# Performance work log

Measured on AMD Instinct MI355X. Metric: run time of the kernel, lower is better.

Reference implementation:

```python
import jax, jax.numpy as jnp
import numpy as np

EPS = 1e-8
VOX_WIDTH = 1.0
CURV_THRESH = 0.5


def _build_kernels():
    """Nine 3x3x3 central finite-difference stencils, pre-divided by vox_width / vox_width^2."""
    def zk():
        return np.zeros((3, 3, 3), np.float32)
    ks = {}
    # first derivatives (central difference), denominator vox_width
    for name, ax in (('ddx', 0), ('ddy', 1), ('ddz', 2)):
        k = zk(); i = [1, 1, 1]
        i[ax] = 0; k[tuple(i)] = -0.5
        i[ax] = 2; k[tuple(i)] = 0.5
        ks[name] = k / VOX_WIDTH
    # pure second derivatives, denominator vox_width^2
    for name, ax in (('d2dx2', 0), ('d2dy2', 1), ('d2dz2', 2)):
        k = zk(); i = [1, 1, 1]
        i[ax] = 0; k[tuple(i)] = 1.0
        i[ax] = 1; k[tuple(i)] = -2.0
        i[ax] = 2; k[tuple(i)] = 1.0
        ks[name] = k / VOX_WIDTH ** 2
    # mixed second derivatives, denominator vox_width^2
    for name, (a, b) in (('d2dxdy', (0, 1)), ('d2dxdz', (0, 2)), ('d2dydz', (1, 2))):
        k = zk()
        for sa, sb, v in ((0, 0, 0.25), (0, 2, -0.25), (2, 0, -0.25), (2, 2, 0.25)):
            i = [1, 1, 1]; i[a] = sa; i[b] = sb; k[tuple(i)] = v
        ks[name] = k / VOX_WIDTH ** 2
    order = ['ddx', 'ddy', 'ddz', 'd2dx2', 'd2dy2', 'd2dz2', 'd2dxdy', 'd2dxdz', 'd2dydz']
    return np.stack([ks[n] for n in order])[:, None]  # [9, 1, 3, 3, 3]


_KERNELS = jnp.asarray(_build_kernels())


def setup_inputs() -> dict:
    key = jax.random.key(0)
    phi = jax.random.normal(key, (2, 1, 192, 192, 192), dtype=jnp.float32)
    return {"phi": phi}


def reference(phi):
    # all nine stencils as one valid 3D conv: [N, 9, D-2, H-2, W-2]
    g = jax.lax.conv_general_dilated(
        phi, _KERNELS, window_strides=(1, 1, 1), padding='VALID',
        dimension_numbers=('NCDHW', 'OIDHW', 'NCDHW'))
    gx, gy, gz, hxx, hyy, hzz, hxy, hxz, hyz = (g[:, i:i + 1] for i in range(9))

    mag = jnp.sqrt(gx * gx + gy * gy + gz * gz + EPS)
    mag3 = mag ** 3

    # mean curvature: sum_{i!=j} g_i^2 H_jj - 2 sum_{i<j} g_i g_j H_ij, over |grad|^3
    cross = gx * gy * hxy + gx * gz * hxz + gy * gz * hyz
    mean_c = (gx * gx * (hyy + hzz) + gy * gy * (hxx + hzz) + gz * gz * (hxx + hyy)
              - 2.0 * cross) / (mag3 + EPS)

    # gaussian curvature: laplacian/|grad| - (g^T H g)/|grad|^3
    lap = (hxx + hyy + hzz) / (mag + EPS)
    quad = (gx * gx * hxx + gy * gy * hyy + gz * gz * hzz + 2.0 * cross) / (mag3 + EPS)
    gauss = lap - quad

    k1 = mean_c + jnp.sqrt(jnp.abs(mean_c ** 2 - gauss) + EPS)
    pen = jax.nn.relu((k1 / (CURV_THRESH + EPS)) ** 2 - 1.0)

    # zero crossings of phi over 3x3x3 neighborhoods (valid -> matches conv output shape)
    mn = jax.lax.reduce_window(phi, jnp.inf, jax.lax.min, (1, 1, 3, 3, 3), (1, 1, 1, 1, 1), 'VALID')
    mx = jax.lax.reduce_window(phi, -jnp.inf, jax.lax.max, (1, 1, 3, 3, 3), (1, 1, 1, 1, 1), 'VALID')
    phi_zero = jax.lax.stop_gradient((mn * mx < 0).astype(phi.dtype))

    return jnp.sum(phi_zero * pen) / (jnp.sum(phi_zero) + EPS)
```

## Files before the change

kernel.cpp:

```cpp
#include <hip/hip_runtime.h>


typedef float v2f __attribute__((ext_vector_type(2)));

constexpr int DIM  = 192;
constexpr int ODIM = 190;
constexpr int TX = 32, TY = 32, CZ = 7;
constexpr int NTX = 6, NTY = 6, NTZ = 28;
constexpr int HX = 34, HY = 34;
constexpr int LX = 36;
constexpr int NELEM = HX * HY;
constexpr int NBLOCKS = 2 * NTZ * NTY * NTX;

struct Slice {
    v2f   q[3][4];
    float mn[6], mx[6];
};

__global__ __launch_bounds__(256, 3) void curv_main(const float* __restrict__ phi,
                                                    double* __restrict__ acc,
                                                    int use_partials) {
    __shared__ __align__(16) float tile[3][HY][LX];

    int bx = blockIdx.x;
    const int tx = bx % NTX; bx /= NTX;
    const int ty = bx % NTY; bx /= NTY;
    const int tz = bx % NTZ; bx /= NTZ;
    const int n  = bx;

    const int xbase = tx * TX, ybase = ty * TY, zbase = tz * CZ;
    const int tid = threadIdx.x;
    const float* pn = phi + (long long)n * DIM * DIM * DIM;

    int goff[5], loff[5];
#pragma unroll
    for (int it = 0; it < 5; ++it) {
        int idx = tid + it * 256; if (idx > NELEM - 1) idx = NELEM - 1;
        int ly = idx / HX, lx = idx - ly * HX;
        int iy = ybase + ly; if (iy > DIM - 1) iy = DIM - 1;
        int ix = xbase + lx; if (ix > DIM - 1) ix = DIM - 1;
        goff[it] = iy * DIM + ix;
        loff[it] = ly * LX + lx;
    }
    const bool st5 = (tid + 1024 < NELEM);

    float pf[5];
    auto pref = [&](int g) {
        int gz = zbase + g; if (gz > DIM - 1) gz = DIM - 1;
        const float* src = pn + gz * DIM * DIM;
#pragma unroll
        for (int it = 0; it < 5; ++it) pf[it] = src[goff[it]];
    };
    float* tf = &tile[0][0][0];
    auto commit = [&](int slot) {
        float* t = tf + slot * (HY * LX);
#pragma unroll
        for (int it = 0; it < 4; ++it) t[loff[it]] = pf[it];
        if (st5) t[loff[4]] = pf[4];
    };

    const int row = tid >> 3;
    const int x0  = (tid & 7) * 4;

    auto read_slice = [&](int slot, Slice& s) {
#pragma unroll
        for (int dy = 0; dy < 3; ++dy) {
            const float* rp = &tile[slot][row + dy][x0];
            const float4 a = *(const float4*)rp;
            const float2 b = *(const float2*)(rp + 4);
            s.q[dy][0] = (v2f){a.x, a.z};
            s.q[dy][1] = (v2f){a.y, a.w};
            s.q[dy][2] = (v2f){a.z, b.x};
            s.q[dy][3] = (v2f){a.w, b.y};
            if (dy == 0) {
                s.mn[0] = a.x; s.mn[1] = a.y; s.mn[2] = a.z;
                s.mn[3] = a.w; s.mn[4] = b.x; s.mn[5] = b.y;
                s.mx[0] = a.x; s.mx[1] = a.y; s.mx[2] = a.z;
                s.mx[3] = a.w; s.mx[4] = b.x; s.mx[5] = b.y;
            } else {
                s.mn[0] = fminf(s.mn[0], a.x); s.mx[0] = fmaxf(s.mx[0], a.x);
                s.mn[1] = fminf(s.mn[1], a.y); s.mx[1] = fmaxf(s.mx[1], a.y);
                s.mn[2] = fminf(s.mn[2], a.z); s.mx[2] = fmaxf(s.mx[2], a.z);
                s.mn[3] = fminf(s.mn[3], a.w); s.mx[3] = fmaxf(s.mx[3], a.w);
                s.mn[4] = fminf(s.mn[4], b.x); s.mx[4] = fmaxf(s.mx[4], b.x);
                s.mn[5] = fminf(s.mn[5], b.y); s.mx[5] = fmaxf(s.mx[5], b.y);
            }
        }
    };

    double sp = 0.0, sc = 0.0;
    const float EPSF = 1e-8f;
    const int oy = ybase + row;

    bool vmask[4];
#pragma unroll
    for (int j = 0; j < 4; ++j)
        vmask[j] = (oy < ODIM) && (xbase + x0 + j < ODIM);

    auto compute = [&](const Slice& s0, const Slice& s1, const Slice& s2, int zo) {
        const int oz = zbase + zo;
        if (oz >= ODIM) return;

        float colmn[6], colmx[6];
#pragma unroll
        for (int c = 0; c < 6; ++c) {
            colmn[c] = fminf(fminf(s0.mn[c], s1.mn[c]), s2.mn[c]);
            colmx[c] = fmaxf(fmaxf(s0.mx[c], s1.mx[c]), s2.mx[c]);
        }

        float fsp = 0.0f, fsc = 0.0f;
#pragma unroll
        for (int p = 0; p < 2; ++p) {
            v2f gx = 0.5f * (s2.q[1][p + 1] - s0.q[1][p + 1]);
            v2f gy = 0.5f * (s1.q[2][p + 1] - s1.q[0][p + 1]);
            v2f gz = 0.5f * (s1.q[1][p + 2] - s1.q[1][p]);

            v2f c2  = 2.0f * s1.q[1][p + 1];
            v2f hxx = s0.q[1][p + 1] - c2 + s2.q[1][p + 1];
            v2f hyy = s1.q[0][p + 1] - c2 + s1.q[2][p + 1];
            v2f hzz = s1.q[1][p] - c2 + s1.q[1][p + 2];

            v2f hxy = 0.25f * (s0.q[0][p + 1] - s0.q[2][p + 1]
                             - s2.q[0][p + 1] + s2.q[2][p + 1]);
            v2f hxz = 0.25f * (s0.q[1][p] - s0.q[1][p + 2]
                             - s2.q[1][p] + s2.q[1][p + 2]);
            v2f hyz = 0.25f * (s1.q[0][p] - s1.q[0][p + 2]
                             - s1.q[2][p] + s1.q[2][p + 2]);

            v2f gx2 = gx * gx, gy2 = gy * gy, gz2 = gz * gz;
            v2f mag2 = gx2 + gy2 + gz2 + EPSF;

            v2f inv1 = (v2f){ __builtin_amdgcn_rsqf(mag2.x),
                              __builtin_amdgcn_rsqf(mag2.y) };
            v2f inv3 = inv1 * inv1 * inv1;

            v2f cross = gx * gy * hxy + gx * gz * hxz + gy * gz * hyz;

            v2f mean_c = (gx2 * (hyy + hzz) + gy2 * (hxx + hzz) +
                          gz2 * (hxx + hyy) - 2.0f * cross) * inv3;
            v2f lap   = (hxx + hyy + hzz) * inv1;
            v2f quad  = (gx2 * hxx + gy2 * hyy + gz2 * hzz + 2.0f * cross) * inv3;
            v2f gauss = lap - quad;

            v2f disc = mean_c * mean_c - gauss;
            v2f sq = (v2f){ sqrtf(fabsf(disc.x) + EPSF),
                            sqrtf(fabsf(disc.y) + EPSF) };
            v2f k1 = mean_c + sq;
            v2f t  = 2.0f * k1;
            v2f pen2 = t * t - 1.0f;

#pragma unroll
            for (int e = 0; e < 2; ++e) {
                const int j = p + 2 * e;
                float pen = fmaxf(e ? pen2.y : pen2.x, 0.0f);
                float mn = fminf(fminf(colmn[j], colmn[j + 1]), colmn[j + 2]);
                float mx = fmaxf(fmaxf(colmx[j], colmx[j + 1]), colmx[j + 2]);
                if (vmask[j] && (mn * mx < 0.0f)) {
                    fsp += pen;
                    fsc += 1.0f;
                }
            }
        }
        sp += (double)fsp;
        sc += (double)fsc;
    };

    Slice s0, s1, s2;

    pref(0); commit(0);
    pref(1); commit(1);
    pref(2);
    __syncthreads();
    read_slice(0, s0);
    read_slice(1, s1);

    commit(2); pref(3); __syncthreads(); read_slice(2, s2); compute(s0, s1, s2, 0);
    commit(0); pref(4); __syncthreads(); read_slice(0, s0); compute(s1, s2, s0, 1);
    commit(1); pref(5); __syncthreads(); read_slice(1, s1); compute(s2, s0, s1, 2);
    commit(2); pref(6); __syncthreads(); read_slice(2, s2); compute(s0, s1, s2, 3);
    commit(0); pref(7); __syncthreads(); read_slice(0, s0); compute(s1, s2, s0, 4);
    commit(1); pref(8); __syncthreads(); read_slice(1, s1); compute(s2, s0, s1, 5);
    commit(2);          __syncthreads(); read_slice(2, s2); compute(s0, s1, s2, 6);

#pragma unroll
    for (int off = 32; off > 0; off >>= 1) {
        sp += __shfl_down(sp, off, 64);
        sc += __shfl_down(sc, off, 64);
    }

    __shared__ double lsp[4], lsc[4];
    const int wave = tid >> 6, lane = tid & 63;
    if (lane == 0) { lsp[wave] = sp; lsc[wave] = sc; }
    __syncthreads();
    if (tid == 0) {
        double tp = lsp[0] + lsp[1] + lsp[2] + lsp[3];
        double tc = lsc[0] + lsc[1] + lsc[2] + lsc[3];
        if (use_partials) {
            acc[2 * blockIdx.x]     = tp;
            acc[2 * blockIdx.x + 1] = tc;
        } else {
            atomicAdd(&acc[0], tp);
            atomicAdd(&acc[1], tc);
        }
    }
}

__global__ __launch_bounds__(256) void curv_reduce(const double* __restrict__ part,
                                                   int nblocks, int use_partials,
                                                   float* __restrict__ out) {
    double sp = 0.0, sc = 0.0;
    if (use_partials) {
        for (int i = threadIdx.x; i < nblocks; i += 256) {
            sp += part[2 * i];
            sc += part[2 * i + 1];
        }
    } else if (threadIdx.x == 0) {
        sp = part[0]; sc = part[1];
    }
#pragma unroll
    for (int off = 32; off > 0; off >>= 1) {
        sp += __shfl_down(sp, off, 64);
        sc += __shfl_down(sc, off, 64);
    }
    __shared__ double lsp[4], lsc[4];
    const int wave = threadIdx.x >> 6, lane = threadIdx.x & 63;
    if (lane == 0) { lsp[wave] = sp; lsc[wave] = sc; }
    __syncthreads();
    if (threadIdx.x == 0) {
        double tp = lsp[0] + lsp[1] + lsp[2] + lsp[3];
        double tc = lsc[0] + lsc[1] + lsc[2] + lsc[3];
        out[0] = (float)(tp / (tc + 1e-8));
    }
}

extern "C" void kernel_launch(void* const* d_in, const int* in_sizes, int n_in,
                              void* d_out, int out_size, void* d_ws, size_t ws_size,
                              hipStream_t stream) {
    const float* phi = (const float*)d_in[0];
    float* out = (float*)d_out;
    double* acc = (double*)d_ws;

    const int use_partials = (ws_size >= (size_t)(2 * NBLOCKS) * sizeof(double)) ? 1 : 0;
    if (!use_partials) {
        hipMemsetAsync(d_ws, 0, 2 * sizeof(double), stream);
    }

    curv_main<<<NBLOCKS, 256, 0, stream>>>(phi, acc, use_partials);
    curv_reduce<<<1, 256, 0, stream>>>(acc, NBLOCKS, use_partials, out);
}
```

Measured before the change: 112.9 us.

## Replace shared-memory slice staging with direct global vector loads per thread

Removes the LDS tile and the per-slice __syncthreads. Each thread now loads its own 3-row float4+float2 window straight from global memory into registers. The z-chunk grows from 7 to 10 outputs so the two-slice halo is amortised over more outputs. Overlapping neighbour reads now rely on L1/L2 caching rather than shared memory, which raises global load traffic; the larger chunk also means fewer blocks and more tail work for the last z tile.

After: 110.9 us. Within noise of the previous version (-1.8%).

```diff
diff --git a/kernel.cpp b/kernel.cpp
--- a/kernel.cpp
+++ b/kernel.cpp
@@ -5,11 +5,9 @@
 
 constexpr int DIM  = 192;
 constexpr int ODIM = 190;
-constexpr int TX = 32, TY = 32, CZ = 7;
-constexpr int NTX = 6, NTY = 6, NTZ = 28;
-constexpr int HX = 34, HY = 34;
-constexpr int LX = 36;
-constexpr int NELEM = HX * HY;
+constexpr int TX = 32, TY = 32, CZ = 10;
+constexpr int NTX = 6, NTY = 6, NTZ = 19;
+constexpr int PLANE = DIM * DIM;
 constexpr int NBLOCKS = 2 * NTZ * NTY * NTX;
 
 struct Slice {
@@ -20,8 +18,6 @@
 __global__ __launch_bounds__(256, 3) void curv_main(const float* __restrict__ phi,
                                                     double* __restrict__ acc,
                                                     int use_partials) {
-    __shared__ __align__(16) float tile[3][HY][LX];
-
     int bx = blockIdx.x;
     const int tx = bx % NTX; bx /= NTX;
     const int ty = bx % NTY; bx /= NTY;
@@ -30,44 +26,35 @@
 
     const int xbase = tx * TX, ybase = ty * TY, zbase = tz * CZ;
     const int tid = threadIdx.x;
-    const float* pn = phi + (long long)n * DIM * DIM * DIM;
-
-    int goff[5], loff[5];
-#pragma unroll
-    for (int it = 0; it < 5; ++it) {
-        int idx = tid + it * 256; if (idx > NELEM - 1) idx = NELEM - 1;
-        int ly = idx / HX, lx = idx - ly * HX;
-        int iy = ybase + ly; if (iy > DIM - 1) iy = DIM - 1;
-        int ix = xbase + lx; if (ix > DIM - 1) ix = DIM - 1;
-        goff[it] = iy * DIM + ix;
-        loff[it] = ly * LX + lx;
-    }
-    const bool st5 = (tid + 1024 < NELEM);
-
-    float pf[5];
+    const int row = tid >> 3;
+    const int x0  = (tid & 7) * 4;
+    const float* pn = phi + (long long)n * DIM * PLANE;
+
+    const int c4 = xbase + x0;
+    int c2t = c4 + 4; if (c2t > DIM - 2) c2t = DIM - 2;
+    const int c2 = c2t;
+    int yoff[3];
+#pragma unroll
+    for (int dy = 0; dy < 3; ++dy) {
+        int iy = ybase + row + dy; if (iy > DIM - 1) iy = DIM - 1;
+        yoff[dy] = iy * DIM;
+    }
+
+    float4 t4[3]; float2 t2[3];
     auto pref = [&](int g) {
         int gz = zbase + g; if (gz > DIM - 1) gz = DIM - 1;
-        const float* src = pn + gz * DIM * DIM;
-#pragma unroll
-        for (int it = 0; it < 5; ++it) pf[it] = src[goff[it]];
+        const float* base = pn + gz * PLANE;
+#pragma unroll
+        for (int dy = 0; dy < 3; ++dy) {
+            t4[dy] = *(const float4*)(base + yoff[dy] + c4);
+            t2[dy] = *(const float2*)(base + yoff[dy] + c2);
+        }
     };
-    float* tf = &tile[0][0][0];
-    auto commit = [&](int slot) {
-        float* t = tf + slot * (HY * LX);
-#pragma unroll
-        for (int it = 0; it < 4; ++it) t[loff[it]] = pf[it];
-        if (st5) t[loff[4]] = pf[4];
-    };
-
-    const int row = tid >> 3;
-    const int x0  = (tid & 7) * 4;
-
-    auto read_slice = [&](int slot, Slice& s) {
+
+    auto unpack = [&](Slice& s) {
 #pragma unroll
         for (int dy = 0; dy < 3; ++dy) {
-            const float* rp = &tile[slot][row + dy][x0];
-            const float4 a = *(const float4*)rp;
-            const float2 b = *(const float2*)(rp + 4);
+            const float4 a = t4[dy]; const float2 b = t2[dy];
             s.q[dy][0] = (v2f){a.x, a.z};
             s.q[dy][1] = (v2f){a.y, a.w};
             s.q[dy][2] = (v2f){a.z, b.x};
@@ -115,10 +102,10 @@
             v2f gy = 0.5f * (s1.q[2][p + 1] - s1.q[0][p + 1]);
             v2f gz = 0.5f * (s1.q[1][p + 2] - s1.q[1][p]);
 
-            v2f c2  = 2.0f * s1.q[1][p + 1];
-            v2f hxx = s0.q[1][p + 1] - c2 + s2.q[1][p + 1];
-            v2f hyy = s1.q[0][p + 1] - c2 + s1.q[2][p + 1];
-            v2f hzz = s1.q[1][p] - c2 + s1.q[1][p + 2];
+            v2f c2v = 2.0f * s1.q[1][p + 1];
+            v2f hxx = s0.q[1][p + 1] - c2v + s2.q[1][p + 1];
+            v2f hyy = s1.q[0][p + 1] - c2v + s1.q[2][p + 1];
+            v2f hzz = s1.q[1][p] - c2v + s1.q[1][p + 2];
 
             v2f hxy = 0.25f * (s0.q[0][p + 1] - s0.q[2][p + 1]
                              - s2.q[0][p + 1] + s2.q[2][p + 1]);
@@ -167,20 +154,20 @@
 
     Slice s0, s1, s2;
 
-    pref(0); commit(0);
-    pref(1); commit(1);
+    pref(0); unpack(s0);
+    pref(1); unpack(s1);
     pref(2);
-    __syncthreads();
-    read_slice(0, s0);
-    read_slice(1, s1);
-
-    commit(2); pref(3); __syncthreads(); read_slice(2, s2); compute(s0, s1, s2, 0);
-    commit(0); pref(4); __syncthreads(); read_slice(0, s0); compute(s1, s2, s0, 1);
-    commit(1); pref(5); __syncthreads(); read_slice(1, s1); compute(s2, s0, s1, 2);
-    commit(2); pref(6); __syncthreads(); read_slice(2, s2); compute(s0, s1, s2, 3);
-    commit(0); pref(7); __syncthreads(); read_slice(0, s0); compute(s1, s2, s0, 4);
-    commit(1); pref(8); __syncthreads(); read_slice(1, s1); compute(s2, s0, s1, 5);
-    commit(2);          __syncthreads(); read_slice(2, s2); compute(s0, s1, s2, 6);
+
+    unpack(s2); pref(3);  compute(s0, s1, s2, 0);
+    unpack(s0); pref(4);  compute(s1, s2, s0, 1);
+    unpack(s1); pref(5);  compute(s2, s0, s1, 2);
+    unpack(s2); pref(6);  compute(s0, s1, s2, 3);
+    unpack(s0); pref(7);  compute(s1, s2, s0, 4);
+    unpack(s1); pref(8);  compute(s2, s0, s1, 5);
+    unpack(s2); pref(9);  compute(s0, s1, s2, 6);
+    unpack(s0); pref(10); compute(s1, s2, s0, 7);
+    unpack(s1); pref(11); compute(s2, s0, s1, 8);
+    unpack(s2);           compute(s0, s1, s2, 9);
 
 #pragma unroll
     for (int off = 32; off > 0; off >>= 1) {
```
